# Kernel tuning notes

Hardware: AMD Instinct MI355X
Metric: run time of the kernel (lower is better)

## Reference

```python
import jax, jax.numpy as jnp
import numpy as np

N, E, IN, H, ED, G, OUT = 50000, 800000, 128, 256, 32, 500, 16
LN_EPS = 1e-5
BN_EPS = 1e-5


def _w(key, shape, scale=0.05):
    return scale * jax.random.normal(key, shape, dtype=jnp.float32)


def setup_inputs() -> dict:
    key = jax.random.key(0)
    ks = iter(jax.random.split(key, 64))
    inp = {
        'x': jax.random.normal(next(ks), (N, IN), jnp.float32),
        'edge_index': jax.random.randint(next(ks), (2, E), 0, N, jnp.int64),
        'edge_attr': jax.random.normal(next(ks), (E, ED), jnp.float32),
        'batch': jnp.sort(jax.random.randint(next(ks), (N,), 0, G, jnp.int64)),
    }
    def conv_params(pfx, din):
        return {
            pfx + '_Wq': _w(next(ks), (din, H)), pfx + '_bq': jnp.zeros((H,), jnp.float32),
            pfx + '_Wk': _w(next(ks), (din, H)), pfx + '_bk': jnp.zeros((H,), jnp.float32),
            pfx + '_Wv': _w(next(ks), (din, H)), pfx + '_bv': jnp.zeros((H,), jnp.float32),
            pfx + '_We': _w(next(ks), (ED, H)),
            pfx + '_Ws': _w(next(ks), (din, H)), pfx + '_bs': jnp.zeros((H,), jnp.float32),
        }
    inp.update(conv_params('conv1', IN))
    inp.update({'ln1_g': jnp.ones((H,), jnp.float32), 'ln1_b': jnp.zeros((H,), jnp.float32)})
    inp.update(conv_params('conv2', H))
    inp.update({'ln2_g': jnp.ones((H,), jnp.float32), 'ln2_b': jnp.zeros((H,), jnp.float32)})
    for pfx in ('gin1', 'gin2'):
        inp.update({
            pfx + '_W1': _w(next(ks), (H, H)), pfx + '_b1': jnp.zeros((H,), jnp.float32),
            pfx + '_bng': jnp.ones((H,), jnp.float32), pfx + '_bnb': jnp.zeros((H,), jnp.float32),
            pfx + '_W2': _w(next(ks), (H, H)), pfx + '_b2': jnp.zeros((H,), jnp.float32),
        })
    inp.update({'lin_W': _w(next(ks), (H, H)), 'lin_b': jnp.zeros((H,), jnp.float32),
                'clf_W': _w(next(ks), (H, OUT)), 'clf_b': jnp.zeros((OUT,), jnp.float32)})
    return inp


def transformer_conv(x, src, dst, ea, Wq, bq, Wk, bk, Wv, bv, We, Ws, bs):
    # PyG TransformerConv, heads=1, edge_dim set, root_weight=True, beta=False
    h = Wq.shape[1]
    q = x @ Wq + bq                      # [N,H]
    e = ea @ We                          # [E,H]
    ke = (x @ Wk + bk)[src] + e          # [E,H]
    ve = (x @ Wv + bv)[src] + e          # [E,H]
    score = jnp.sum(q[dst] * ke, axis=-1) / jnp.sqrt(jnp.float32(h))  # [E]
    m = jax.ops.segment_max(score, dst, num_segments=N)
    ex = jnp.exp(score - m[dst])
    denom = jax.ops.segment_sum(ex, dst, num_segments=N)
    alpha = ex / (denom[dst] + 1e-16)
    out = jax.ops.segment_sum(alpha[:, None] * ve, dst, num_segments=N)
    return out + x @ Ws + bs


def layer_norm(x, g, b):
    mu = jnp.mean(x, axis=-1, keepdims=True)
    var = jnp.var(x, axis=-1, keepdims=True)
    return (x - mu) * jax.lax.rsqrt(var + LN_EPS) * g + b


def gin_conv(x, src, dst, W1, b1, bng, bnb, W2, b2):
    # GINConv(eps=0): mlp(x + sum_{j in N(i)} x_j); MLP = Linear-BN-ReLU-Linear
    agg = jax.ops.segment_sum(x[src], dst, num_segments=N)
    h = x + agg
    y = h @ W1 + b1
    mu = jnp.mean(y, axis=0)
    var = jnp.var(y, axis=0)
    y = (y - mu) * jax.lax.rsqrt(var + BN_EPS) * bng + bnb
    y = jax.nn.relu(y)
    return y @ W2 + b2


def reference(x, edge_index, edge_attr, batch,
              conv1_Wq, conv1_bq, conv1_Wk, conv1_bk, conv1_Wv, conv1_bv, conv1_We, conv1_Ws, conv1_bs,
              ln1_g, ln1_b,
              conv2_Wq, conv2_bq, conv2_Wk, conv2_bk, conv2_Wv, conv2_bv, conv2_We, conv2_Ws, conv2_bs,
              ln2_g, ln2_b,
              gin1_W1, gin1_b1, gin1_bng, gin1_bnb, gin1_W2, gin1_b2,
              gin2_W1, gin2_b1, gin2_bng, gin2_bnb, gin2_W2, gin2_b2,
              lin_W, lin_b, clf_W, clf_b):
    src, dst = edge_index[0], edge_index[1]
    # NodeEncoder (dropout inactive in eval)
    h = transformer_conv(x, src, dst, edge_attr, conv1_Wq, conv1_bq, conv1_Wk, conv1_bk,
                         conv1_Wv, conv1_bv, conv1_We, conv1_Ws, conv1_bs)
    h = layer_norm(jax.nn.leaky_relu(h), ln1_g, ln1_b)
    h = transformer_conv(h, src, dst, edge_attr, conv2_Wq, conv2_bq, conv2_Wk, conv2_bk,
                         conv2_Wv, conv2_bv, conv2_We, conv2_Ws, conv2_bs)
    h = layer_norm(jax.nn.leaky_relu(h), ln2_g, ln2_b)
    # GIN_Net, max_depth=2: conv -> relu -> conv
    h = gin_conv(h, src, dst, gin1_W1, gin1_b1, gin1_bng, gin1_bnb, gin1_W2, gin1_b2)
    h = jax.nn.relu(h)
    h = gin_conv(h, src, dst, gin2_W1, gin2_b1, gin2_bng, gin2_bnb, gin2_W2, gin2_b2)
    # global_add_pool + MLP head
    pooled = jax.ops.segment_sum(h, batch, num_segments=G)   # [G,H]
    z = jax.nn.relu(pooled @ lin_W + lin_b)
    return z @ clf_W + clf_b                                 # [G,OUT]
```

## Files before the change

### kernel.cpp

```cpp
#include <hip/hip_runtime.h>
#include <math.h>

#define NN 50000
#define NE 800000
#define DIN 128
#define DH 256
#define DED 32
#define NG 500
#define DOUT 16
#define SCAN_T 256

typedef __bf16 bf16_t;
typedef __bf16 bf16x4 __attribute__((ext_vector_type(4)));
typedef __bf16 bf16x8 __attribute__((ext_vector_type(8)));
typedef float f32x4 __attribute__((ext_vector_type(4)));

__device__ __forceinline__ void async_copy16(const bf16_t* g, bf16_t* l) {
  __builtin_amdgcn_global_load_lds(
      (const __attribute__((address_space(1))) void*)g,
      (__attribute__((address_space(3))) void*)l, 16, 0, 0);
}

__global__ void fill_i32(int* __restrict__ p, int v, int n) {
  int i = blockIdx.x * 256 + threadIdx.x;
  if (i < n) p[i] = v;
}
__global__ void cast_bf16x8_k(const float* __restrict__ in, bf16_t* __restrict__ o, long n8) {
  long i = (long)blockIdx.x * 256 + threadIdx.x;
  if (i >= n8) return;
  const f32x4* sp = (const f32x4*)&in[i * 8];
  f32x4 a = __builtin_nontemporal_load(sp);
  f32x4 b = __builtin_nontemporal_load(sp + 1);
  bf16x8 r;
#pragma unroll
  for (int j = 0; j < 4; ++j) { r[j] = (bf16_t)a[j]; r[j + 4] = (bf16_t)b[j]; }
  *(bf16x8*)&o[i * 8] = r;
}

__global__ void count_k(const int* __restrict__ dst, int* __restrict__ deg) {
  int e = blockIdx.x * 256 + threadIdx.x;
  if (e < NE) atomicAdd(&deg[dst[e]], 1);
}
__global__ void scan1(const int* __restrict__ deg, int* __restrict__ rowptr,
                      int* __restrict__ bsum, int n) {
  __shared__ int s[SCAN_T];
  int t = threadIdx.x, i = blockIdx.x * SCAN_T + t;
  int v = (i < n) ? deg[i] : 0;
  s[t] = v; __syncthreads();
  for (int off = 1; off < SCAN_T; off <<= 1) {
    int add = (t >= off) ? s[t - off] : 0;
    __syncthreads(); s[t] += add; __syncthreads();
  }
  if (i < n) rowptr[i + 1] = s[t];
  if (t == SCAN_T - 1) bsum[blockIdx.x] = s[t];
}
__global__ void scan2(const int* __restrict__ bsum, int* __restrict__ boff, int nb) {
  __shared__ int s[SCAN_T];
  int t = threadIdx.x;
  int v = (t < nb) ? bsum[t] : 0;
  s[t] = v; __syncthreads();
  for (int off = 1; off < SCAN_T; off <<= 1) {
    int add = (t >= off) ? s[t - off] : 0;
    __syncthreads(); s[t] += add; __syncthreads();
  }
  boff[t] = s[t] - v;
}
__global__ void scan3(int* __restrict__ rowptr, const int* __restrict__ boff, int n) {
  int i = blockIdx.x * 256 + threadIdx.x;
  if (i < n) rowptr[i + 1] += boff[i >> 8];
  if (i == 0) rowptr[0] = 0;
}
__global__ void scatter_k(const int* __restrict__ dst, const int* __restrict__ src,
                          const int* __restrict__ rowptr, int* __restrict__ cursor,
                          int* __restrict__ esrc, int* __restrict__ epos) {
  int e = blockIdx.x * 256 + threadIdx.x;
  if (e < NE) {
    int d = dst[e];
    int pos = rowptr[d] + atomicAdd(&cursor[d], 1);
    esrc[pos] = src[e];
    epos[e] = pos;
  }
}
__global__ void permute_ea(const int* __restrict__ epos, const float* __restrict__ ea,
                           bf16_t* __restrict__ eac) {
  long t = (long)blockIdx.x * 256 + threadIdx.x;
  if (t >= (long)NE * 4) return;
  int e = (int)(t >> 2), c8 = ((int)t & 3) * 8;
  int pos = epos[e];
  const f32x4* sp = (const f32x4*)&ea[(size_t)e * DED + c8];
  f32x4 a = __builtin_nontemporal_load(sp);
  f32x4 b = __builtin_nontemporal_load(sp + 1);
  bf16x8 o;
#pragma unroll
  for (int j = 0; j < 4; ++j) { o[j] = (bf16_t)a[j]; o[j + 4] = (bf16_t)b[j]; }
  __builtin_nontemporal_store(o, (bf16x8*)&eac[(size_t)pos * DED + c8]);
}

struct PackEnt { const float* src; bf16_t* dst; int K; int N; };
struct PackArgs { PackEnt e[16]; };
__global__ void pack_all(PackArgs pa) {
  PackEnt en = pa.e[blockIdx.y];
  int i = blockIdx.x * 256 + threadIdx.x;
  if (i >= en.K * en.N) return;
  int el = i & 511, f = i >> 9;
  int ntiles = en.N >> 4;
  int ks = f / ntiles, t = f - ks * ntiles;
  int lane = el >> 3, j = el & 7;
  int k = ks * 32 + (lane >> 4) * 8 + j;
  int n = t * 16 + (lane & 15);
  en.dst[i] = (bf16_t)en.src[(size_t)k * en.N + n];
}

__global__ void wqe_k(const float* __restrict__ Wq, const float* __restrict__ We,
                      const float* __restrict__ bq, float* __restrict__ Wqe,
                      float* __restrict__ bqe, int din) {
  int idx = blockIdx.x * 256 + threadIdx.x;
  if (idx < din * 32) {
    int d = idx >> 5, j = idx & 31;
    float s = 0.f;
    for (int h = 0; h < DH; ++h) s += Wq[(size_t)d * DH + h] * We[(size_t)j * DH + h];
    Wqe[idx] = s;
  }
  if (idx < 32) {
    float s = 0.f;
    for (int h = 0; h < DH; ++h) s += bq[h] * We[(size_t)idx * DH + h];
    bqe[idx] = s;
  }
}

template<int NT, int RT>
__device__ __forceinline__ void gemm_body(
    const bf16_t* __restrict__ Ab, const bf16_t* __restrict__ Wp,
    const float* __restrict__ bias, float* __restrict__ Cf, bf16_t* __restrict__ Cb,
    int M, int K, int relu, int rstride, int bx,
    float* __restrict__ psum, float* __restrict__ psq)
{
  __shared__ bf16_t Atile[2][RT * 2048];
  __shared__ bf16_t Btile[2][NT * 512];
  const int ACH = RT * 256;
  const int NCH = ACH + NT * 64;
  int tid = threadIdx.x;
  int lane = tid & 63, wv = tid >> 6;
  int base = bx * (RT * 64);
  f32x4 acc[RT][NT];
#pragma unroll
  for (int rt = 0; rt < RT; ++rt)
#pragma unroll
    for (int t = 0; t < NT; ++t) acc[rt][t] = (f32x4){0.f, 0.f, 0.f, 0.f};
  int arow = wv * (16 * RT) + (lane & 15);
  int aq = (lane >> 4) * 8;
  int nk = K >> 5;

  auto stage = [&](int buf, int ks) {
    for (int c = tid; c < NCH; c += 256) {
      if (c < ACH) {
        int r = c >> 2, qq = c & 3;
        async_copy16(Ab + (size_t)(base + r) * K + ks * 32 + qq * 8,
                     &Atile[buf][c * 8]);
      } else {
        int cb = c - ACH;
        async_copy16(Wp + (size_t)ks * NT * 512 + cb * 8, &Btile[buf][cb * 8]);
      }
    }
  };

  stage(0, 0);
  asm volatile("s_waitcnt vmcnt(0)" ::: "memory");
  __builtin_amdgcn_s_barrier();
  int cur = 0;
  for (int ks = 0; ks < nk; ++ks) {
    if (ks + 1 < nk) stage(cur ^ 1, ks + 1);
    bf16x8 a[RT];
#pragma unroll
    for (int rt = 0; rt < RT; ++rt)
      a[rt] = *(const bf16x8*)&Atile[cur][(arow + rt * 16) * 32 + aq];
#pragma unroll
    for (int t = 0; t < NT; ++t) {
      bf16x8 b = *(const bf16x8*)&Btile[cur][t * 512 + lane * 8];
#pragma unroll
      for (int rt = 0; rt < RT; ++rt)
        acc[rt][t] = __builtin_amdgcn_mfma_f32_16x16x32_bf16(a[rt], b, acc[rt][t], 0, 0, 0);
    }
    asm volatile("s_waitcnt vmcnt(0)" ::: "memory");
    __builtin_amdgcn_s_barrier();
    cur ^= 1;
  }
  int col_l = lane & 15;
#pragma unroll
  for (int rt = 0; rt < RT; ++rt) {
    int rbase = base + wv * (16 * RT) + rt * 16 + (lane >> 4) * 4;
#pragma unroll
    for (int t = 0; t < NT; ++t) {
      int col = t * 16 + col_l;
      float bv = bias ? bias[col] : 0.f;
#pragma unroll
      for (int r = 0; r < 4; ++r) {
        int row = rbase + r;
        if (row >= M) continue;
        float vv = acc[rt][t][r] + bv;
        if (relu) vv = fmaxf(vv, 0.f);
        if (Cf) Cf[(size_t)row * rstride + col] = vv;
        if (Cb) Cb[(size_t)row * rstride + col] = (bf16_t)vv;
      }
    }
  }
  if (psum) {
#pragma unroll
    for (int t = 0; t < NT; ++t) {
      float sc = 0.f, sq = 0.f;
      float bv = bias[t * 16 + col_l];
#pragma unroll
      for (int rt = 0; rt < RT; ++rt) {
        int rbase = base + wv * (16 * RT) + rt * 16 + (lane >> 4) * 4;
#pragma unroll
        for (int r = 0; r < 4; ++r) {
          if (rbase + r >= M) continue;
          float vv = acc[rt][t][r] + bv;
          sc += vv; sq += vv * vv;
        }
      }
      sc += __shfl_xor(sc, 16, 64); sc += __shfl_xor(sc, 32, 64);
      sq += __shfl_xor(sq, 16, 64); sq += __shfl_xor(sq, 32, 64);
      if (lane < 16) {
        int col = t * 16 + lane;
        atomicAdd(&psum[wv * DH + col], sc);
        atomicAdd(&psq[wv * DH + col], sq);
      }
    }
  }
}

template<int NT>
__global__ __launch_bounds__(256, 3) void gemm_r1(
    const bf16_t* __restrict__ Ab, const bf16_t* __restrict__ Wp,
    const float* __restrict__ bias, float* __restrict__ Cf, bf16_t* __restrict__ Cb,
    int M, int K, int relu, int rstride, float* psum, float* psq)
{
  gemm_body<NT, 1>(Ab, Wp, bias, Cf, Cb, M, K, relu, rstride, blockIdx.x, psum, psq);
}

struct QkvsArgs { const bf16_t* w[4]; const float* bias[4]; bf16_t* outp[4]; };
__global__ __launch_bounds__(256, 3) void gemm_qkvs(
    const bf16_t* __restrict__ Ab, QkvsArgs qa, int M, int K)
{
  int which = blockIdx.y;
  gemm_body<16, 2>(Ab, qa.w[which], qa.bias[which], nullptr, qa.outp[which], M, K, 0, 1024,
                   blockIdx.x, nullptr, nullptr);
}

__global__ __launch_bounds__(256) void conv_edge_fused(
    const int* __restrict__ rowptr, const int* __restrict__ esrc,
    const bf16_t* __restrict__ qkvs, const bf16_t* __restrict__ eac,
    const float* __restrict__ QEf,
    bf16_t* __restrict__ AGGn, bf16_t* __restrict__ EAn)
{
  int l = threadIdx.x & 31;
  int half = (threadIdx.x >> 5) & 1;
  int n = blockIdx.x * 4 + (threadIdx.x >> 6);
  if (n >= NN) return;
  float q[8];
  {
    bf16x8 t = __builtin_nontemporal_load((const bf16x8*)&qkvs[(size_t)n * 1024 + l * 8]);
#pragma unroll
    for (int j = 0; j < 8; ++j) q[j] = (float)t[j];
  }
  float qe[8];
#pragma unroll
  for (int j = 0; j < 8; ++j) qe[j] = 0.f;
  if (l < 4) {
    const f32x4* p = (const f32x4*)&QEf[(size_t)n * DED + l * 8];
    f32x4 qa = __builtin_nontemporal_load(p);
    f32x4 qb = __builtin_nontemporal_load(p + 1);
#pragma unroll
    for (int j = 0; j < 4; ++j) { qe[j] = qa[j]; qe[j + 4] = qb[j]; }
  }
  float s = 0.f;
  float acc[8], eacc[8];
#pragma unroll
  for (int j = 0; j < 8; ++j) { acc[j] = 0.f; eacc[j] = 0.f; }
  int i0 = rowptr[n], i1 = rowptr[n + 1];
  for (int wb = i0; wb < i1; wb += 32) {
    int wcnt = min(32, i1 - wb);
    int widx = (l < wcnt) ? esrc[wb + l] : 0;
    int e = 0;
    for (; e + 8 <= wcnt; e += 8) {
      int s1 = __shfl(widx, e + half, 32);
      int s2 = __shfl(widx, e + 2 + half, 32);
      int s3 = __shfl(widx, e + 4 + half, 32);
      int s4 = __shfl(widx, e + 6 + half, 32);
      const bf16_t* b1 = &qkvs[(size_t)s1 * 1024 + 256 + l * 8];
      const bf16_t* b2 = &qkvs[(size_t)s2 * 1024 + 256 + l * 8];
      const bf16_t* b3 = &qkvs[(size_t)s3 * 1024 + 256 + l * 8];
      const bf16_t* b4 = &qkvs[(size_t)s4 * 1024 + 256 + l * 8];
      bf16x8 k1 = *(const bf16x8*)b1;
      bf16x8 k2 = *(const bf16x8*)b2;
      bf16x8 k3 = *(const bf16x8*)b3;
      bf16x8 k4 = *(const bf16x8*)b4;
      bf16x8 v1 = *(const bf16x8*)(b1 + 256);
      bf16x8 v2 = *(const bf16x8*)(b2 + 256);
      bf16x8 v3 = *(const bf16x8*)(b3 + 256);
      bf16x8 v4 = *(const bf16x8*)(b4 + 256);
      bf16x8 t1 = {}, t2 = {}, t3 = {}, t4 = {};
      if (l < 4) {
        const bf16_t* ep = &eac[(size_t)(wb + e + half) * DED + l * 8];
        t1 = __builtin_nontemporal_load((const bf16x8*)ep);
        t2 = __builtin_nontemporal_load((const bf16x8*)(ep + 2 * DED));
        t3 = __builtin_nontemporal_load((const bf16x8*)(ep + 4 * DED));
        t4 = __builtin_nontemporal_load((const bf16x8*)(ep + 6 * DED));
      }
      float p1 = 0.f, p2 = 0.f, p3 = 0.f, p4 = 0.f;
#pragma unroll
      for (int j = 0; j < 8; ++j) {
        p1 = fmaf(q[j], (float)k1[j], p1);
        p2 = fmaf(q[j], (float)k2[j], p2);
        p3 = fmaf(q[j], (float)k3[j], p3);
        p4 = fmaf(q[j], (float)k4[j], p4);
      }
#pragma unroll
      for (int j = 0; j < 8; ++j) {
        p1 = fmaf(qe[j], (float)t1[j], p1);
        p2 = fmaf(qe[j], (float)t2[j], p2);
        p3 = fmaf(qe[j], (float)t3[j], p3);
        p4 = fmaf(qe[j], (float)t4[j], p4);
      }
#pragma unroll
      for (int off = 16; off > 0; off >>= 1) {
        p1 += __shfl_xor(p1, off, 32);
        p2 += __shfl_xor(p2, off, 32);
        p3 += __shfl_xor(p3, off, 32);
        p4 += __shfl_xor(p4, off, 32);
      }
      float ex1 = __expf(p1 * 0.0625f);
      float ex2 = __expf(p2 * 0.0625f);
      float ex3 = __expf(p3 * 0.0625f);
      float ex4 = __expf(p4 * 0.0625f);
      s += (ex1 + ex2) + (ex3 + ex4);
#pragma unroll
      for (int j = 0; j < 8; ++j) {
        acc[j] = fmaf(ex1, (float)v1[j], acc[j]);
        acc[j] = fmaf(ex2, (float)v2[j], acc[j]);
        acc[j] = fmaf(ex3, (float)v3[j], acc[j]);
        acc[j] = fmaf(ex4, (float)v4[j], acc[j]);
      }
#pragma unroll
      for (int j = 0; j < 8; ++j) {
        eacc[j] = fmaf(ex1, (float)t1[j], eacc[j]);
        eacc[j] = fmaf(ex2, (float)t2[j], eacc[j]);
        eacc[j] = fmaf(ex3, (float)t3[j], eacc[j]);
        eacc[j] = fmaf(ex4, (float)t4[j], eacc[j]);
      }
    }
    for (; e < wcnt; e += 2) {
      int eh = e + half;
      bool act = eh < wcnt;
      int s1 = __shfl(widx, act ? eh : e, 32);
      const bf16_t* b1 = &qkvs[(size_t)s1 * 1024 + 256 + l * 8];
      bf16x8 k1 = *(const bf16x8*)b1;
      bf16x8 v1 = *(const bf16x8*)(b1 + 256);
      bf16x8 t1 = {};
      if (act && l < 4)
        t1 = __builtin_nontemporal_load((const bf16x8*)&eac[(size_t)(wb + eh) * DED + l * 8]);
      float p1 = 0.f;
#pragma unroll
      for (int j = 0; j < 8; ++j) p1 = fmaf(q[j], (float)k1[j], p1);
#pragma unroll
      for (int j = 0; j < 8; ++j) p1 = fmaf(qe[j], (float)t1[j], p1);
#pragma unroll
      for (int off = 16; off > 0; off >>= 1) p1 += __shfl_xor(p1, off, 32);
      float ex1 = act ? __expf(p1 * 0.0625f) : 0.f;
      s += ex1;
#pragma unroll
      for (int j = 0; j < 8; ++j) acc[j] = fmaf(ex1, (float)v1[j], acc[j]);
#pragma unroll
      for (int j = 0; j < 8; ++j) eacc[j] = fmaf(ex1, (float)t1[j], eacc[j]);
    }
  }
  s += __shfl_xor(s, 32, 64);
#pragma unroll
  for (int j = 0; j < 8; ++j) acc[j] += __shfl_xor(acc[j], 32, 64);
#pragma unroll
  for (int j = 0; j < 8; ++j) eacc[j] += __shfl_xor(eacc[j], 32, 64);
  float inv = 1.f / (s + 1e-16f);
  if (half == 0) {
    bf16x8 o;
#pragma unroll
    for (int j = 0; j < 8; ++j) o[j] = (bf16_t)(acc[j] * inv);
    __builtin_nontemporal_store(o, (bf16x8*)&AGGn[(size_t)n * DH + l * 8]);
    if (l < 4) {
      bf16x8 eo;
#pragma unroll
      for (int j = 0; j < 8; ++j) eo[j] = (bf16_t)(eacc[j] * inv);
      __builtin_nontemporal_store(eo, (bf16x8*)&EAn[(size_t)n * DED + l * 8]);
    }
  }
}

__global__ __launch_bounds__(256) void conv_epilogue(
    const bf16_t* __restrict__ AGGn, const bf16_t* __restrict__ E2N,
    const bf16_t* __restrict__ qkvs, const float* __restrict__ g,
    const float* __restrict__ b, bf16_t* __restrict__ out)
{
  int wv = threadIdx.x >> 6, lane = threadIdx.x & 63;
  int n = blockIdx.x * 4 + wv;
  if (n >= NN) return;
  size_t base = (size_t)n * DH + lane * 4;
  bf16x4 a = __builtin_nontemporal_load((const bf16x4*)&AGGn[base]);
  bf16x4 e2 = __builtin_nontemporal_load((const bf16x4*)&E2N[base]);
  bf16x4 sv = __builtin_nontemporal_load(
      (const bf16x4*)&qkvs[(size_t)n * 1024 + 768 + lane * 4]);
  float v[4];
#pragma unroll
  for (int j = 0; j < 4; ++j) {
    float t = (float)a[j] + (float)e2[j] + (float)sv[j];
    v[j] = (t > 0.f) ? t : 0.01f * t;
  }
  float sum = v[0] + v[1] + v[2] + v[3];
  float sq = v[0]*v[0] + v[1]*v[1] + v[2]*v[2] + v[3]*v[3];
#pragma unroll
  for (int off = 32; off > 0; off >>= 1) {
    sum += __shfl_xor(sum, off, 64);
    sq  += __shfl_xor(sq, off, 64);
  }
  float mu = sum * (1.f / DH);
  float var = sq * (1.f / DH) - mu * mu;
  float rstd = rsqrtf(var + 1e-5f);
  bf16x4 o;
#pragma unroll
  for (int j = 0; j < 4; ++j)
    o[j] = (bf16_t)((v[j] - mu) * rstd * g[lane * 4 + j] + b[lane * 4 + j]);
  *(bf16x4*)&out[base] = o;
}

__global__ __launch_bounds__(256) void gin_gather(
    const int* __restrict__ rowptr, const int* __restrict__ esrc,
    const bf16_t* __restrict__ h, bf16_t* __restrict__ out)
{
  int l = threadIdx.x & 31;
  int half = (threadIdx.x >> 5) & 1;
  int n = blockIdx.x * 4 + (threadIdx.x >> 6);
  if (n >= NN) return;
  size_t co = (size_t)n * DH + l * 8;
  float acc[8];
  {
    bf16x8 hv = *(const bf16x8*)&h[co];
    float w0 = (half == 0) ? 1.f : 0.f;
#pragma unroll
    for (int j = 0; j < 8; ++j) acc[j] = w0 * (float)hv[j];
  }
  int i0 = rowptr[n], i1 = rowptr[n + 1];
  for (int wb = i0; wb < i1; wb += 32) {
    int wcnt = min(32, i1 - wb);
    int widx = (l < wcnt) ? esrc[wb + l] : 0;
    int e = 0;
    for (; e + 8 <= wcnt; e += 8) {
      int s1 = __shfl(widx, e + half, 32);
      int s2 = __shfl(widx, e + 2 + half, 32);
      int s3 = __shfl(widx, e + 4 + half, 32);
      int s4 = __shfl(widx, e + 6 + half, 32);
      bf16x8 t1 = *(const bf16x8*)&h[(size_t)s1 * DH + l * 8];
      bf16x8 t2 = *(const bf16x8*)&h[(size_t)s2 * DH + l * 8];
      bf16x8 t3 = *(const bf16x8*)&h[(size_t)s3 * DH + l * 8];
      bf16x8 t4 = *(const bf16x8*)&h[(size_t)s4 * DH + l * 8];
#pragma unroll
      for (int j = 0; j < 8; ++j)
        acc[j] += ((float)t1[j] + (float)t2[j]) + ((float)t3[j] + (float)t4[j]);
    }
    for (; e < wcnt; e += 2) {
      int eh = e + half;
      bool act = eh < wcnt;
      int s1 = __shfl(widx, act ? eh : e, 32);
      bf16x8 t1 = *(const bf16x8*)&h[(size_t)s1 * DH + l * 8];
      float w = act ? 1.f : 0.f;
#pragma unroll
      for (int j = 0; j < 8; ++j) acc[j] += w * (float)t1[j];
    }
  }
#pragma unroll
  for (int j = 0; j < 8; ++j) acc[j] += __shfl_xor(acc[j], 32, 64);
  if (half == 0) {
    bf16x8 o;
#pragma unroll
    for (int j = 0; j < 8; ++j) o[j] = (bf16_t)acc[j];
    __builtin_nontemporal_store(o, (bf16x8*)&out[co]);
  }
}

__global__ void bn_final_na(const float* __restrict__ psum, const float* __restrict__ psq,
                            const float* __restrict__ bng, const float* __restrict__ bnb,
                            float* __restrict__ scale, float* __restrict__ shift) {
  int c = threadIdx.x;
  float s = 0.f, ss = 0.f;
  for (int b = 0; b < 4; ++b) { s += psum[b * DH + c]; ss += psq[b * DH + c]; }
  float mu = s * (1.f / NN);
  float var = ss * (1.f / NN) - mu * mu;
  float rstd = rsqrtf(var + 1e-5f);
  float sc = bng[c] * rstd;
  scale[c] = sc;
  shift[c] = bnb[c] - mu * sc;
}
__global__ void bn_apply_relu8(const bf16_t* __restrict__ y, const float* __restrict__ scale,
                               const float* __restrict__ shift, bf16_t* __restrict__ o, int n8) {
  int i = blockIdx.x * 256 + threadIdx.x;
  if (i >= n8) return;
  bf16x8 v = __builtin_nontemporal_load((const bf16x8*)&y[(size_t)i * 8]);
  int c = (i * 8) & (DH - 1);
  bf16x8 r;
#pragma unroll
  for (int j = 0; j < 8; ++j)
    r[j] = (bf16_t)fmaxf((float)v[j] * scale[c + j] + shift[c + j], 0.f);
  *(bf16x8*)&o[(size_t)i * 8] = r;
}

__global__ __launch_bounds__(256) void pool_sorted(
    const int* __restrict__ batch, const bf16_t* __restrict__ h, float* __restrict__ pooled)
{
  __shared__ int s0, s1;
  int g = blockIdx.x;
  if (threadIdx.x == 0) {
    int lo = 0, hi = NN;
    while (lo < hi) { int mid = (lo + hi) >> 1; if (batch[mid] < g) lo = mid + 1; else hi = mid; }
    s0 = lo;
  }
  if (threadIdx.x == 1) {
    int lo = 0, hi = NN;
    while (lo < hi) { int mid = (lo + hi) >> 1; if (batch[mid] < g + 1) lo = mid + 1; else hi = mid; }
    s1 = lo;
  }
  __syncthreads();
  int c = threadIdx.x;
  float acc = 0.f;
  for (int r = s0; r < s1; ++r)
    acc += (float)__builtin_nontemporal_load(&h[(size_t)r * DH + c]);
  pooled[(size_t)g * DH + c] = acc;
}

__global__ __launch_bounds__(256) void gemm_bias_act(
    const float* __restrict__ A, const float* __restrict__ Wm,
    const float* __restrict__ bias, float* __restrict__ C,
    int M, int K, int Ncol, int act)
{
  __shared__ __align__(16) float As[16][68];
  __shared__ __align__(16) float Bs[16][68];
  int tid = threadIdx.x;
  int tx = tid & 15, ty = tid >> 4;
  int row0 = blockIdx.y * 64 + ty * 4;
  int col0 = blockIdx.x * 64 + tx * 4;
  float acc[4][4] = {{0.f}};
  for (int k0 = 0; k0 < K; k0 += 16) {
#pragma unroll
    for (int l = 0; l < 4; ++l) {
      int e = tid + l * 256;
      int r = e >> 4, kk = e & 15;
      int gr = blockIdx.y * 64 + r;
      As[kk][r] = (gr < M) ? A[(size_t)gr * K + k0 + kk] : 0.f;
    }
#pragma unroll
    for (int l = 0; l < 4; ++l) {
      int e = tid + l * 256;
      int kk = e >> 6, c = e & 63;
      int gc = blockIdx.x * 64 + c;
      Bs[kk][c] = (gc < Ncol) ? Wm[(size_t)(k0 + kk) * Ncol + gc] : 0.f;
    }
    __syncthreads();
#pragma unroll
    for (int kk = 0; kk < 16; ++kk) {
      float4 a4 = *(const float4*)&As[kk][ty * 4];
      float4 b4 = *(const float4*)&Bs[kk][tx * 4];
      float a[4] = {a4.x, a4.y, a4.z, a4.w};
      float b[4] = {b4.x, b4.y, b4.z, b4.w};
#pragma unroll
      for (int i = 0; i < 4; ++i)
#pragma unroll
        for (int j = 0; j < 4; ++j)
          acc[i][j] = fmaf(a[i], b[j], acc[i][j]);
    }
    __syncthreads();
  }
#pragma unroll
  for (int i = 0; i < 4; ++i) {
    int r = row0 + i;
    if (r >= M) continue;
#pragma unroll
    for (int j = 0; j < 4; ++j) {
      int c = col0 + j;
      if (c >= Ncol) continue;
      float val = acc[i][j];
      if (bias) val += bias[c];
      if (act == 1) val = fmaxf(val, 0.f);
      C[(size_t)r * Ncol + c] = val;
    }
  }
}

static inline void launch_filli(hipStream_t st, int* p, int v, long n) {
  fill_i32<<<dim3((unsigned)((n + 255) / 256)), dim3(256), 0, st>>>(p, v, (int)n);
}

extern "C" void kernel_launch(void* const* d_in, const int* in_sizes, int n_in,
                              void* d_out, int out_size, void* d_ws, size_t ws_size,
                              hipStream_t stream) {
  const float* x  = (const float*)d_in[0];
  const int* ei   = (const int*)d_in[1];
  const float* ea = (const float*)d_in[2];
  const int* batch = (const int*)d_in[3];
  const int* src = ei;
  const int* dst = ei + NE;

  const float* c1[9]; for (int i = 0; i < 9; ++i) c1[i] = (const float*)d_in[4 + i];
  const float* ln1g = (const float*)d_in[13]; const float* ln1b = (const float*)d_in[14];
  const float* c2[9]; for (int i = 0; i < 9; ++i) c2[i] = (const float*)d_in[15 + i];
  const float* ln2g = (const float*)d_in[24]; const float* ln2b = (const float*)d_in[25];
  const float* g1[6]; for (int i = 0; i < 6; ++i) g1[i] = (const float*)d_in[26 + i];
  const float* g2[6]; for (int i = 0; i < 6; ++i) g2[i] = (const float*)d_in[32 + i];
  const float* linW = (const float*)d_in[38]; const float* linb = (const float*)d_in[39];
  const float* clfW = (const float*)d_in[40]; const float* clfb = (const float*)d_in[41];
  float* out = (float*)d_out;

  size_t off = 0;
  auto alloc = [&](size_t bytes) -> void* {
    void* r = (char*)d_ws + off;
    off += (bytes + 255) & ~(size_t)255;
    return r;
  };
  int* deg    = (int*)alloc(NN * 4);
  int* cursor = (int*)alloc(NN * 4);
  int* rowptr = (int*)alloc((NN + 1) * 4);
  int* esrc   = (int*)alloc((size_t)NE * 4);
  int* epos   = (int*)alloc((size_t)NE * 4);
  int* bsum   = (int*)alloc(1024);
  int* boff   = (int*)alloc(1024);
  float* QEf   = (float*)alloc((size_t)NN * DED * 4);
  float* pooled = (float*)alloc((size_t)NG * DH * 4);
  float* zbuf   = (float*)alloc((size_t)NG * DH * 4);
  float* psum  = (float*)alloc(4 * DH * 4);
  float* psq   = (float*)alloc(4 * DH * 4);
  float* bnscale = (float*)alloc(DH * 4);
  float* bnshift = (float*)alloc(DH * 4);
  float* wqe_tmp1 = (float*)alloc((size_t)DIN * DED * 4);
  float* wqe_tmp2 = (float*)alloc((size_t)DH * DED * 4);
  float* bqe1 = (float*)alloc(DED * 4);
  float* bqe2 = (float*)alloc(DED * 4);
  bf16_t* qkvsb = (bf16_t*)alloc((size_t)NN * 1024 * 2);
  bf16_t* h_b = (bf16_t*)alloc((size_t)NN * DH * 2);
  bf16_t* g_b = (bf16_t*)alloc((size_t)NN * DH * 2);
  bf16_t* Yb  = (bf16_t*)alloc((size_t)NN * DH * 2);
  bf16_t* AGGb = (bf16_t*)alloc((size_t)NN * DH * 2);
  bf16_t* E2Nb = (bf16_t*)alloc((size_t)NN * DH * 2);
  bf16_t* EAn = (bf16_t*)alloc((size_t)NN * DED * 2);
  bf16_t* xb  = (bf16_t*)alloc((size_t)NN * DIN * 2);
  bf16_t* eac = (bf16_t*)alloc((size_t)NE * DED * 2);
  bf16_t* Hb = (bf16_t*)qkvsb;
  bf16_t* pk1q = (bf16_t*)alloc(DIN * DH * 2);
  bf16_t* pk1k = (bf16_t*)alloc(DIN * DH * 2);
  bf16_t* pk1v = (bf16_t*)alloc(DIN * DH * 2);
  bf16_t* pk1s = (bf16_t*)alloc(DIN * DH * 2);
  bf16_t* pk1qe = (bf16_t*)alloc(DIN * DED * 2);
  bf16_t* pk1we = (bf16_t*)alloc(DED * DH * 2);
  bf16_t* pk2q = (bf16_t*)alloc(DH * DH * 2);
  bf16_t* pk2k = (bf16_t*)alloc(DH * DH * 2);
  bf16_t* pk2v = (bf16_t*)alloc(DH * DH * 2);
  bf16_t* pk2s = (bf16_t*)alloc(DH * DH * 2);
  bf16_t* pk2qe = (bf16_t*)alloc(DH * DED * 2);
  bf16_t* pk2we = (bf16_t*)alloc(DED * DH * 2);
  bf16_t* pkg1a = (bf16_t*)alloc(DH * DH * 2);
  bf16_t* pkg1b = (bf16_t*)alloc(DH * DH * 2);
  bf16_t* pkg2a = (bf16_t*)alloc(DH * DH * 2);
  bf16_t* pkg2b = (bf16_t*)alloc(DH * DH * 2);
  if (ws_size < off) return;

  const int GRID_M  = (NN + 127) / 128;
  const int GRID_M1 = (NN + 63) / 64;

  cast_bf16x8_k<<<dim3((unsigned)(((long)NN * DIN / 8 + 255) / 256)), dim3(256), 0, stream>>>(
      x, xb, (long)NN * DIN / 8);
  wqe_k<<<dim3((DIN * 32 + 255) / 256), dim3(256), 0, stream>>>(c1[0], c1[6], c1[1], wqe_tmp1, bqe1, DIN);
  wqe_k<<<dim3((DH * 32 + 255) / 256), dim3(256), 0, stream>>>(c2[0], c2[6], c2[1], wqe_tmp2, bqe2, DH);
  PackArgs pa;
  pa.e[0]  = {c1[0], pk1q, DIN, DH};
  pa.e[1]  = {c1[2], pk1k, DIN, DH};
  pa.e[2]  = {c1[4], pk1v, DIN, DH};
  pa.e[3]  = {c1[7], pk1s, DIN, DH};
  pa.e[4]  = {c1[6], pk1we, DED, DH};
  pa.e[5]  = {wqe_tmp1, pk1qe, DIN, DED};
  pa.e[6]  = {c2[0], pk2q, DH, DH};
  pa.e[7]  = {c2[2], pk2k, DH, DH};
  pa.e[8]  = {c2[4], pk2v, DH, DH};
  pa.e[9]  = {c2[7], pk2s, DH, DH};
  pa.e[10] = {c2[6], pk2we, DED, DH};
  pa.e[11] = {wqe_tmp2, pk2qe, DH, DED};
  pa.e[12] = {g1[0], pkg1a, DH, DH};
  pa.e[13] = {g1[4], pkg1b, DH, DH};
  pa.e[14] = {g2[0], pkg2a, DH, DH};
  pa.e[15] = {g2[4], pkg2b, DH, DH};
  pack_all<<<dim3(256, 16), dim3(256), 0, stream>>>(pa);

  const int nb1 = (NN + SCAN_T - 1) / SCAN_T;
  launch_filli(stream, deg, 0, 2 * ((NN * 4 + 255) & ~255) / 4);
  count_k<<<dim3((NE + 255) / 256), dim3(256), 0, stream>>>(dst, deg);
  scan1<<<dim3(nb1), dim3(SCAN_T), 0, stream>>>(deg, rowptr, bsum, NN);
  scan2<<<dim3(1), dim3(SCAN_T), 0, stream>>>(bsum, boff, nb1);
  scan3<<<dim3(nb1), dim3(SCAN_T), 0, stream>>>(rowptr, boff, NN);
  scatter_k<<<dim3((NE + 255) / 256), dim3(256), 0, stream>>>(dst, src, rowptr, cursor, esrc, epos);
  permute_ea<<<dim3((unsigned)(((long)NE * 4 + 255) / 256)), dim3(256), 0, stream>>>(epos, ea, eac);

  auto conv = [&](const bf16_t* Ain, int K,
                  const bf16_t* pq, const bf16_t* pk, const bf16_t* pv, const bf16_t* ps,
                  const bf16_t* pqe, const bf16_t* pwe,
                  const float* const* P, const float* bqe,
                  const float* lng, const float* lnb, bf16_t* outb) {
    QkvsArgs qa;
    qa.w[0] = pq; qa.w[1] = pk; qa.w[2] = pv; qa.w[3] = ps;
    qa.bias[0] = P[1]; qa.bias[1] = P[3]; qa.bias[2] = P[5]; qa.bias[3] = P[8];
    qa.outp[0] = qkvsb + 0; qa.outp[1] = qkvsb + 256;
    qa.outp[2] = qkvsb + 512; qa.outp[3] = qkvsb + 768;
    gemm_qkvs<<<dim3(GRID_M, 4), dim3(256), 0, stream>>>(Ain, qa, NN, K);
    gemm_r1<2><<<dim3(GRID_M1), dim3(256), 0, stream>>>(
        Ain, pqe, bqe, QEf, nullptr, NN, K, 0, 32, nullptr, nullptr);
    conv_edge_fused<<<dim3((NN + 3) / 4), dim3(256), 0, stream>>>(
        rowptr, esrc, qkvsb, eac, QEf, AGGb, EAn);
    gemm_r1<16><<<dim3(GRID_M1), dim3(256), 0, stream>>>(
        EAn, pwe, nullptr, nullptr, E2Nb, NN, DED, 0, 256, nullptr, nullptr);
    conv_epilogue<<<dim3((NN + 3) / 4), dim3(256), 0, stream>>>(
        AGGb, E2Nb, qkvsb, lng, lnb, outb);
  };

  auto gin = [&](const bf16_t* hin, const bf16_t* pw1, const bf16_t* pw2,
                 const float* const* P, int relu_out, bf16_t* outb) {
    gin_gather<<<dim3((NN + 3) / 4), dim3(256), 0, stream>>>(rowptr, esrc, hin, g_b);
    launch_filli(stream, (int*)psum, 0, 2 * 4 * DH);
    gemm_r1<16><<<dim3(GRID_M1), dim3(256), 0, stream>>>(
        g_b, pw1, P[1], nullptr, Yb, NN, DH, 0, 256, psum, psq);
    bn_final_na<<<dim3(1), dim3(256), 0, stream>>>(psum, psq, P[2], P[3], bnscale, bnshift);
    bn_apply_relu8<<<dim3((NN * DH / 8 + 255) / 256), dim3(256), 0, stream>>>(
        Yb, bnscale, bnshift, g_b, NN * DH / 8);
    gemm_r1<16><<<dim3(GRID_M1), dim3(256), 0, stream>>>(
        g_b, pw2, P[5], nullptr, outb, NN, DH, relu_out, 256, nullptr, nullptr);
  };

  conv(xb, DIN, pk1q, pk1k, pk1v, pk1s, pk1qe, pk1we, c1, bqe1, ln1g, ln1b, h_b);
  conv(h_b, DH, pk2q, pk2k, pk2v, pk2s, pk2qe, pk2we, c2, bqe2, ln2g, ln2b, h_b);
  gin(h_b, pkg1a, pkg1b, g1, 1, h_b);
  gin(h_b, pkg2a, pkg2b, g2, 0, Hb);

  pool_sorted<<<dim3(NG), dim3(256), 0, stream>>>(batch, Hb, pooled);
  gemm_bias_act<<<dim3(4, 8), dim3(256), 0, stream>>>(pooled, linW, linb, zbuf, NG, DH, DH, 1);
  gemm_bias_act<<<dim3(1, 8), dim3(256), 0, stream>>>(zbuf, clfW, clfb, out, NG, DH, DOUT, 0);
}
```

Measured before the change: 1.280 ms.

## Fuse edge-attr projection GEMM into conv epilogue and swap qkvs grid order

Removes the separate GEMM that projected the aggregated edge attributes (EAn) by We into an E2N buffer. The conv epilogue now keeps We in shared memory and computes the 32-wide dot products inline per node, using a persistent grid-stride loop. This avoids writing and re-reading an NN x 256 bf16 intermediate and one kernel launch per conv layer, at the cost of scalar FMA work in the epilogue. It also swaps the qkvs GEMM grid so the four weight matrices for the same row tile are adjacent blocks, which may improve L2 reuse of the A tile.

```diff
diff --git a/kernel.cpp b/kernel.cpp
--- a/kernel.cpp
+++ b/kernel.cpp
@@ -243,9 +243,9 @@
 __global__ __launch_bounds__(256, 3) void gemm_qkvs(
     const bf16_t* __restrict__ Ab, QkvsArgs qa, int M, int K)
 {
-  int which = blockIdx.y;
+  int which = blockIdx.x;
   gemm_body<16, 2>(Ab, qa.w[which], qa.bias[which], nullptr, qa.outp[which], M, K, 0, 1024,
-                   blockIdx.x, nullptr, nullptr);
+                   blockIdx.y, nullptr, nullptr);
 }
 
 __global__ __launch_bounds__(256) void conv_edge_fused(
@@ -396,39 +396,60 @@
 }
 
 __global__ __launch_bounds__(256) void conv_epilogue(
-    const bf16_t* __restrict__ AGGn, const bf16_t* __restrict__ E2N,
-    const bf16_t* __restrict__ qkvs, const float* __restrict__ g,
-    const float* __restrict__ b, bf16_t* __restrict__ out)
+    const bf16_t* __restrict__ AGGn, const bf16_t* __restrict__ EAn,
+    const bf16_t* __restrict__ Web, const bf16_t* __restrict__ qkvs,
+    const float* __restrict__ g, const float* __restrict__ b,
+    bf16_t* __restrict__ out)
 {
-  int wv = threadIdx.x >> 6, lane = threadIdx.x & 63;
-  int n = blockIdx.x * 4 + wv;
-  if (n >= NN) return;
-  size_t base = (size_t)n * DH + lane * 4;
-  bf16x4 a = __builtin_nontemporal_load((const bf16x4*)&AGGn[base]);
-  bf16x4 e2 = __builtin_nontemporal_load((const bf16x4*)&E2N[base]);
-  bf16x4 sv = __builtin_nontemporal_load(
-      (const bf16x4*)&qkvs[(size_t)n * 1024 + 768 + lane * 4]);
-  float v[4];
-#pragma unroll
-  for (int j = 0; j < 4; ++j) {
-    float t = (float)a[j] + (float)e2[j] + (float)sv[j];
-    v[j] = (t > 0.f) ? t : 0.01f * t;
-  }
-  float sum = v[0] + v[1] + v[2] + v[3];
-  float sq = v[0]*v[0] + v[1]*v[1] + v[2]*v[2] + v[3]*v[3];
-#pragma unroll
-  for (int off = 32; off > 0; off >>= 1) {
-    sum += __shfl_xor(sum, off, 64);
-    sq  += __shfl_xor(sq, off, 64);
-  }
-  float mu = sum * (1.f / DH);
-  float var = sq * (1.f / DH) - mu * mu;
-  float rstd = rsqrtf(var + 1e-5f);
-  bf16x4 o;
-#pragma unroll
-  for (int j = 0; j < 4; ++j)
-    o[j] = (bf16_t)((v[j] - mu) * rstd * g[lane * 4 + j] + b[lane * 4 + j]);
-  *(bf16x4*)&out[base] = o;
+  __shared__ bf16_t We_s[DED * DH];
+  int tid = threadIdx.x;
+  for (int i = tid; i < DED * DH / 8; i += 256)
+    *(bf16x8*)&We_s[i * 8] = *(const bf16x8*)&Web[i * 8];
+  __syncthreads();
+  int wv = tid >> 6, lane = tid & 63;
+  float gc[4], bc[4];
+#pragma unroll
+  for (int j = 0; j < 4; ++j) { gc[j] = g[lane * 4 + j]; bc[j] = b[lane * 4 + j]; }
+  for (int n = blockIdx.x * 4 + wv; n < NN; n += gridDim.x * 4) {
+    size_t base = (size_t)n * DH + lane * 4;
+    bf16x4 a = __builtin_nontemporal_load((const bf16x4*)&AGGn[base]);
+    bf16x4 sv = __builtin_nontemporal_load(
+        (const bf16x4*)&qkvs[(size_t)n * 1024 + 768 + lane * 4]);
+    float e2[4] = {0.f, 0.f, 0.f, 0.f};
+    const bf16x8* ep = (const bf16x8*)&EAn[(size_t)n * DED];
+#pragma unroll
+    for (int kb = 0; kb < 4; ++kb) {
+      bf16x8 ev = __builtin_nontemporal_load(ep + kb);
+#pragma unroll
+      for (int k = 0; k < 8; ++k) {
+        float e = (float)ev[k];
+        bf16x4 w = *(const bf16x4*)&We_s[(kb * 8 + k) * DH + lane * 4];
+#pragma unroll
+        for (int j = 0; j < 4; ++j) e2[j] = fmaf(e, (float)w[j], e2[j]);
+      }
+    }
+    float v[4];
+#pragma unroll
+    for (int j = 0; j < 4; ++j) {
+      float t = (float)a[j] + e2[j] + (float)sv[j];
+      v[j] = (t > 0.f) ? t : 0.01f * t;
+    }
+    float sum = v[0] + v[1] + v[2] + v[3];
+    float sq = v[0]*v[0] + v[1]*v[1] + v[2]*v[2] + v[3]*v[3];
+#pragma unroll
+    for (int off = 32; off > 0; off >>= 1) {
+      sum += __shfl_xor(sum, off, 64);
+      sq  += __shfl_xor(sq, off, 64);
+    }
+    float mu = sum * (1.f / DH);
+    float var = sq * (1.f / DH) - mu * mu;
+    float rstd = rsqrtf(var + 1e-5f);
+    bf16x4 o;
+#pragma unroll
+    for (int j = 0; j < 4; ++j)
+      o[j] = (bf16_t)((v[j] - mu) * rstd * gc[j] + bc[j]);
+    *(bf16x4*)&out[base] = o;
+  }
 }
 
 __global__ __launch_bounds__(256) void gin_gather(
@@ -645,7 +666,6 @@
   bf16_t* g_b = (bf16_t*)alloc((size_t)NN * DH * 2);
   bf16_t* Yb  = (bf16_t*)alloc((size_t)NN * DH * 2);
   bf16_t* AGGb = (bf16_t*)alloc((size_t)NN * DH * 2);
-  bf16_t* E2Nb = (bf16_t*)alloc((size_t)NN * DH * 2);
   bf16_t* EAn = (bf16_t*)alloc((size_t)NN * DED * 2);
   bf16_t* xb  = (bf16_t*)alloc((size_t)NN * DIN * 2);
   bf16_t* eac = (bf16_t*)alloc((size_t)NE * DED * 2);
@@ -655,17 +675,17 @@
   bf16_t* pk1v = (bf16_t*)alloc(DIN * DH * 2);
   bf16_t* pk1s = (bf16_t*)alloc(DIN * DH * 2);
   bf16_t* pk1qe = (bf16_t*)alloc(DIN * DED * 2);
-  bf16_t* pk1we = (bf16_t*)alloc(DED * DH * 2);
   bf16_t* pk2q = (bf16_t*)alloc(DH * DH * 2);
   bf16_t* pk2k = (bf16_t*)alloc(DH * DH * 2);
   bf16_t* pk2v = (bf16_t*)alloc(DH * DH * 2);
   bf16_t* pk2s = (bf16_t*)alloc(DH * DH * 2);
   bf16_t* pk2qe = (bf16_t*)alloc(DH * DED * 2);
-  bf16_t* pk2we = (bf16_t*)alloc(DED * DH * 2);
   bf16_t* pkg1a = (bf16_t*)alloc(DH * DH * 2);
   bf16_t* pkg1b = (bf16_t*)alloc(DH * DH * 2);
   bf16_t* pkg2a = (bf16_t*)alloc(DH * DH * 2);
   bf16_t* pkg2b = (bf16_t*)alloc(DH * DH * 2);
+  bf16_t* web1 = (bf16_t*)alloc(DED * DH * 2);
+  bf16_t* web2 = (bf16_t*)alloc(DED * DH * 2);
   if (ws_size < off) return;
 
   const int GRID_M  = (NN + 127) / 128;
@@ -673,6 +693,8 @@
 
   cast_bf16x8_k<<<dim3((unsigned)(((long)NN * DIN / 8 + 255) / 256)), dim3(256), 0, stream>>>(
       x, xb, (long)NN * DIN / 8);
+  cast_bf16x8_k<<<dim3(4), dim3(256), 0, stream>>>(c1[6], web1, DED * DH / 8);
+  cast_bf16x8_k<<<dim3(4), dim3(256), 0, stream>>>(c2[6], web2, DED * DH / 8);
   wqe_k<<<dim3((DIN * 32 + 255) / 256), dim3(256), 0, stream>>>(c1[0], c1[6], c1[1], wqe_tmp1, bqe1, DIN);
   wqe_k<<<dim3((DH * 32 + 255) / 256), dim3(256), 0, stream>>>(c2[0], c2[6], c2[1], wqe_tmp2, bqe2, DH);
   PackArgs pa;
@@ -680,19 +702,19 @@
   pa.e[1]  = {c1[2], pk1k, DIN, DH};
   pa.e[2]  = {c1[4], pk1v, DIN, DH};
   pa.e[3]  = {c1[7], pk1s, DIN, DH};
-  pa.e[4]  = {c1[6], pk1we, DED, DH};
-  pa.e[5]  = {wqe_tmp1, pk1qe, DIN, DED};
-  pa.e[6]  = {c2[0], pk2q, DH, DH};
-  pa.e[7]  = {c2[2], pk2k, DH, DH};
-  pa.e[8]  = {c2[4], pk2v, DH, DH};
-  pa.e[9]  = {c2[7], pk2s, DH, DH};
-  pa.e[10] = {c2[6], pk2we, DED, DH};
-  pa.e[11] = {wqe_tmp2, pk2qe, DH, DED};
-  pa.e[12] = {g1[0], pkg1a, DH, DH};
-  pa.e[13] = {g1[4], pkg1b, DH, DH};
-  pa.e[14] = {g2[0], pkg2a, DH, DH};
-  pa.e[15] = {g2[4], pkg2b, DH, DH};
-  pack_all<<<dim3(256, 16), dim3(256), 0, stream>>>(pa);
+  pa.e[4]  = {wqe_tmp1, pk1qe, DIN, DED};
+  pa.e[5]  = {c2[0], pk2q, DH, DH};
+  pa.e[6]  = {c2[2], pk2k, DH, DH};
+  pa.e[7]  = {c2[4], pk2v, DH, DH};
+  pa.e[8]  = {c2[7], pk2s, DH, DH};
+  pa.e[9]  = {wqe_tmp2, pk2qe, DH, DED};
+  pa.e[10] = {g1[0], pkg1a, DH, DH};
+  pa.e[11] = {g1[4], pkg1b, DH, DH};
+  pa.e[12] = {g2[0], pkg2a, DH, DH};
+  pa.e[13] = {g2[4], pkg2b, DH, DH};
+  pa.e[14] = {nullptr, nullptr, 0, 0};
+  pa.e[15] = {nullptr, nullptr, 0, 0};
+  pack_all<<<dim3(256, 14), dim3(256), 0, stream>>>(pa);
 
   const int nb1 = (NN + SCAN_T - 1) / SCAN_T;
   launch_filli(stream, deg, 0, 2 * ((NN * 4 + 255) & ~255) / 4);
@@ -705,7 +727,7 @@
 
   auto conv = [&](const bf16_t* Ain, int K,
                   const bf16_t* pq, const bf16_t* pk, const bf16_t* pv, const bf16_t* ps,
-                  const bf16_t* pqe, const bf16_t* pwe,
+                  const bf16_t* pqe, const bf16_t* web,
                   const float* const* P, const float* bqe,
                   const float* lng, const float* lnb, bf16_t* outb) {
     QkvsArgs qa;
@@ -713,15 +735,13 @@
     qa.bias[0] = P[1]; qa.bias[1] = P[3]; qa.bias[2] = P[5]; qa.bias[3] = P[8];
     qa.outp[0] = qkvsb + 0; qa.outp[1] = qkvsb + 256;
     qa.outp[2] = qkvsb + 512; qa.outp[3] = qkvsb + 768;
-    gemm_qkvs<<<dim3(GRID_M, 4), dim3(256), 0, stream>>>(Ain, qa, NN, K);
+    gemm_qkvs<<<dim3(4, GRID_M), dim3(256), 0, stream>>>(Ain, qa, NN, K);
     gemm_r1<2><<<dim3(GRID_M1), dim3(256), 0, stream>>>(
         Ain, pqe, bqe, QEf, nullptr, NN, K, 0, 32, nullptr, nullptr);
     conv_edge_fused<<<dim3((NN + 3) / 4), dim3(256), 0, stream>>>(
         rowptr, esrc, qkvsb, eac, QEf, AGGb, EAn);
-    gemm_r1<16><<<dim3(GRID_M1), dim3(256), 0, stream>>>(
-        EAn, pwe, nullptr, nullptr, E2Nb, NN, DED, 0, 256, nullptr, nullptr);
-    conv_epilogue<<<dim3((NN + 3) / 4), dim3(256), 0, stream>>>(
-        AGGb, E2Nb, qkvsb, lng, lnb, outb);
+    conv_epilogue<<<dim3(1024), dim3(256), 0, stream>>>(
+        AGGb, EAn, web, qkvsb, lng, lnb, outb);
   };
 
   auto gin = [&](const bf16_t* hin, const bf16_t* pw1, const bf16_t* pw2,
@@ -737,8 +757,8 @@
         g_b, pw2, P[5], nullptr, outb, NN, DH, relu_out, 256, nullptr, nullptr);
   };
 
-  conv(xb, DIN, pk1q, pk1k, pk1v, pk1s, pk1qe, pk1we, c1, bqe1, ln1g, ln1b, h_b);
-  conv(h_b, DH, pk2q, pk2k, pk2v, pk2s, pk2qe, pk2we, c2, bqe2, ln2g, ln2b, h_b);
+  conv(xb, DIN, pk1q, pk1k, pk1v, pk1s, pk1qe, web1, c1, bqe1, ln1g, ln1b, h_b);
+  conv(h_b, DH, pk2q, pk2k, pk2v, pk2s, pk2qe, web2, c2, bqe2, ln2g, ln2b, h_b);
   gin(h_b, pkg1a, pkg1b, g1, 1, h_b);
   gin(h_b, pkg2a, pkg2b, g2, 0, Hb);
 
```

Result: no change. 1.289 ms (+0.7%).
